# Kernel optimization log

Hardware: AMD Instinct MI355X
Metric: run time of the kernel (lower is better)

## Reference

```python
import jax, jax.numpy as jnp
import numpy as np

V = 500000
VD = 256
G = 4000
H = 8
GD = 256
HIDDEN = 128


def setup_inputs() -> dict:
    key = jax.random.key(0)
    ks = jax.random.split(key, 6)
    node_embeddings = jax.random.normal(ks[0], (V, VD), dtype=jnp.float32)
    node_to_graph_map = jnp.sort(jax.random.randint(ks[1], (V,), 0, G, dtype=jnp.int32))
    scale = lambda fan_in: 1.0 / np.sqrt(fan_in)
    scoring_w1 = jax.random.normal(ks[2], (VD, HIDDEN), dtype=jnp.float32) * scale(VD)
    scoring_w2 = jax.random.normal(ks[3], (HIDDEN, H), dtype=jnp.float32) * scale(HIDDEN)
    transform_w1 = jax.random.normal(ks[4], (VD, HIDDEN), dtype=jnp.float32) * scale(VD)
    transform_w2 = jax.random.normal(ks[5], (HIDDEN, GD), dtype=jnp.float32) * scale(HIDDEN)
    return {
        "node_embeddings": node_embeddings,
        "node_to_graph_map": node_to_graph_map,
        "num_graphs": G,
        "scoring_w1": scoring_w1,
        "scoring_w2": scoring_w2,
        "transform_w1": transform_w1,
        "transform_w2": transform_w2,
    }


def _segment_softmax(logits, segment_ids, num_segments):
    # logits: [V, H]; softmax over nodes within each graph, per head.
    seg_max = jax.ops.segment_max(logits, segment_ids, num_segments=num_segments)
    seg_max = jnp.where(jnp.isfinite(seg_max), seg_max, 0.0)
    exp = jnp.exp(logits - seg_max[segment_ids])
    denom = jax.ops.segment_sum(exp, segment_ids, num_segments=num_segments)
    return exp / denom[segment_ids]


def reference(node_embeddings, node_to_graph_map, num_graphs,
              scoring_w1, scoring_w2, transform_w1, transform_w2):
    # Scoring MLP (hidden ReLU, linear out, no biases): [V, H]
    scores = jax.nn.relu(node_embeddings @ scoring_w1) @ scoring_w2
    # Per-graph softmax weights, per head: [V, H]
    weights = _segment_softmax(scores, node_to_graph_map, num_graphs)
    # Transformation MLP, then the call() applies the activation to the MLP output.
    node_reprs = jax.nn.relu(jax.nn.relu(node_embeddings @ transform_w1) @ transform_w2)  # [V, GD]
    node_reprs = node_reprs.reshape(-1, H, GD // H)  # [V, H, GD/H]
    weighted = (weights[:, :, None] * node_reprs).reshape(-1, GD)  # [V, GD]
    graph_reprs = jax.ops.segment_sum(weighted, node_to_graph_map, num_segments=num_graphs)
    return graph_reprs
```

## Files before the change

### kernel.cpp

```cpp
#include <hip/hip_runtime.h>
#include <hip/hip_fp16.h>

#define VD 256
#define HID 128
#define GD 256
#define NH 8
#define NGRAPH 4000
#define RT 64
#define MAXROWS 512

typedef _Float16 f16;
typedef f16 f16x4 __attribute__((ext_vector_type(4)));
typedef f16 f16x8 __attribute__((ext_vector_type(8)));
typedef float f32x4 __attribute__((ext_vector_type(4)));

__device__ __forceinline__ f16x8 load_a_frag(const float* p) {
  float4 p0 = *(const float4*)(p);
  float4 p1 = *(const float4*)(p + 4);
  f16x8 v;
  v[0] = (f16)p0.x; v[1] = (f16)p0.y; v[2] = (f16)p0.z; v[3] = (f16)p0.w;
  v[4] = (f16)p1.x; v[5] = (f16)p1.y; v[6] = (f16)p1.z; v[7] = (f16)p1.w;
  return v;
}

__device__ __forceinline__ void pack_b_dev(const float* __restrict__ src,
                                           f16* __restrict__ dst,
                                           int K, int Nsrc, int Ndst, int t) {
  int NB = Ndst / 16, KB = K / 32;
  int total = KB * NB * 64;
  if (t >= total) return;
  int lane = t & 63;
  int frag = t >> 6;
  int nb = frag % NB, kb = frag / NB;
  int col = nb * 16 + (lane & 15);
  int krow = kb * 32 + (lane >> 4) * 8;
  f16x8 o;
  #pragma unroll
  for (int i = 0; i < 8; ++i) {
    float v = (col < Nsrc) ? src[(size_t)(krow + i) * Nsrc + col] : 0.0f;
    o[i] = (f16)v;
  }
  *(f16x8*)(dst + (size_t)t * 8) = o;
}

__global__ __launch_bounds__(256) void k_prep(
    const float* __restrict__ w1s, const float* __restrict__ w1t,
    const float* __restrict__ w2t, const float* __restrict__ w2s,
    const int* __restrict__ map,
    f16* __restrict__ W1sp, f16* __restrict__ W1tp,
    f16* __restrict__ W2tp, f16* __restrict__ W2sp,
    int* __restrict__ gs, int V, int G) {
  int b = blockIdx.x;
  int tid = threadIdx.x;
  if (b < 16) {
    pack_b_dev(w1s, W1sp, VD, HID, HID, b * 256 + tid);
  } else if (b < 32) {
    pack_b_dev(w1t, W1tp, VD, HID, HID, (b - 16) * 256 + tid);
  } else if (b < 48) {
    pack_b_dev(w2t, W2tp, HID, GD, GD, (b - 32) * 256 + tid);
  } else if (b == 48) {
    pack_b_dev(w2s, W2sp, HID, NH, 16, tid);
  } else {
    int g = (b - 49) * 256 + tid;
    if (g > G) return;
    int lo = 0, hi = V;
    while (lo < hi) {
      int mid = (lo + hi) >> 1;
      if (map[mid] < g) lo = mid + 1; else hi = mid;
    }
    gs[g] = lo;
  }
}

__global__ __attribute__((amdgpu_flat_work_group_size(512, 512),
                          amdgpu_waves_per_eu(4, 4))) void k_stage1(
    const float* __restrict__ E, int V, int ntiles,
    const f16* __restrict__ W1sp, const f16* __restrict__ W2sp,
    const f16* __restrict__ W1tp,
    float* __restrict__ scores, f16* __restrict__ ht) {
  __shared__ __attribute__((aligned(16))) f16 lE[RT][VD + 8];
  __shared__ __attribute__((aligned(16))) f16 lH[RT][HID + 8];
  __shared__ __attribute__((aligned(16))) f16 lT[RT][HID + 8];
  const int tid = threadIdx.x;
  const int wave = tid >> 6;
  const int lane = tid & 63;
  const int hi = lane >> 4;
  const int lo = lane & 15;
  const int srow = tid >> 6;
  const int scol = (tid & 63) * 4;

  f16x8 Bs[8], Bt[8];
  #pragma unroll
  for (int kb = 0; kb < 8; ++kb) {
    Bs[kb] = *(const f16x8*)(W1sp + ((size_t)(kb * 8 + wave) * 64 + lane) * 8);
    Bt[kb] = *(const f16x8*)(W1tp + ((size_t)(kb * 8 + wave) * 64 + lane) * 8);
  }

  int t = blockIdx.x;
  if (t >= ntiles) return;
  const int stride = gridDim.x;

  float4 pf[8];
  {
    const int r0 = t * RT;
    #pragma unroll
    for (int p = 0; p < 8; ++p) {
      int grow = r0 + p * 8 + srow;
      pf[p] = (grow < V) ? *(const float4*)(E + (size_t)grow * VD + scol)
                         : make_float4(0.f, 0.f, 0.f, 0.f);
    }
  }

  while (t < ntiles) {
    const int r0 = t * RT;
    #pragma unroll
    for (int p = 0; p < 8; ++p) {
      f16x4 h;
      h[0] = (f16)pf[p].x; h[1] = (f16)pf[p].y;
      h[2] = (f16)pf[p].z; h[3] = (f16)pf[p].w;
      *(f16x4*)&lE[p * 8 + srow][scol] = h;
    }
    const int tn = t + stride;
    if (tn < ntiles) {
      const int rn = tn * RT;
      #pragma unroll
      for (int p = 0; p < 8; ++p) {
        int grow = rn + p * 8 + srow;
        pf[p] = (grow < V) ? *(const float4*)(E + (size_t)grow * VD + scol)
                           : make_float4(0.f, 0.f, 0.f, 0.f);
      }
    }
    __syncthreads();

    #pragma unroll
    for (int m = 0; m < 4; ++m) {
      f32x4 as = {0.f, 0.f, 0.f, 0.f};
      f32x4 at = {0.f, 0.f, 0.f, 0.f};
      #pragma unroll
      for (int kb = 0; kb < 8; ++kb) {
        f16x8 a = *(const f16x8*)&lE[m * 16 + lo][kb * 32 + hi * 8];
        as = __builtin_amdgcn_mfma_f32_16x16x32_f16(a, Bs[kb], as, 0, 0, 0);
        at = __builtin_amdgcn_mfma_f32_16x16x32_f16(a, Bt[kb], at, 0, 0, 0);
      }
      #pragma unroll
      for (int r = 0; r < 4; ++r) {
        lH[m * 16 + hi * 4 + r][wave * 16 + lo] = (f16)fmaxf(as[r], 0.f);
        if (ht != nullptr)
          lT[m * 16 + hi * 4 + r][wave * 16 + lo] = (f16)fmaxf(at[r], 0.f);
      }
    }
    __syncthreads();

    if (ht != nullptr) {
      #pragma unroll
      for (int p = 0; p < 2; ++p) {
        int c = p * 512 + tid;
        int row = c >> 4;
        int col = (c & 15) * 8;
        int grow = r0 + row;
        if (grow < V)
          *(f16x8*)(ht + (size_t)grow * HID + col) = *(const f16x8*)&lT[row][col];
      }
    }

    if (wave < 4) {
      f16x8 a2[4];
      #pragma unroll
      for (int kb = 0; kb < 4; ++kb)
        a2[kb] = *(const f16x8*)&lH[wave * 16 + lo][kb * 32 + hi * 8];
      f32x4 acc = {0.f, 0.f, 0.f, 0.f};
      #pragma unroll
      for (int kb = 0; kb < 4; ++kb) {
        f16x8 b = *(const f16x8*)(W2sp + ((size_t)kb * 64 + lane) * 8);
        acc = __builtin_amdgcn_mfma_f32_16x16x32_f16(a2[kb], b, acc, 0, 0, 0);
      }
      if (lo < NH) {
        #pragma unroll
        for (int r = 0; r < 4; ++r) {
          int row = r0 + wave * 16 + hi * 4 + r;
          if (row < V) scores[(size_t)row * NH + lo] = acc[r];
        }
      }
    }
    t = tn;
  }
}

__global__ __attribute__((amdgpu_flat_work_group_size(256, 256),
                          amdgpu_waves_per_eu(4, 4))) void k_graph(
    const f16* __restrict__ ht, const float* __restrict__ scores,
    const f16* __restrict__ W2tp, const int* __restrict__ gs,
    float* __restrict__ out, int V) {
  __shared__ float red[4][NH];
  __shared__ float lW[MAXROWS * NH];
  const int g = blockIdx.x;
  const int tid = threadIdx.x;
  const int wave = tid >> 6;
  const int lane = tid & 63;
  const int hi = lane >> 4;
  const int lo = lane & 15;
  const int s = gs[g], e = gs[g + 1];
  const int n = e - s;

  if (n <= 0) {
    out[(size_t)g * GD + tid] = 0.f;
    return;
  }

  f16x8 b[4][4];
  #pragma unroll
  for (int j = 0; j < 4; ++j)
    #pragma unroll
    for (int kb = 0; kb < 4; ++kb)
      b[j][kb] = *(const f16x8*)(
          W2tp + ((size_t)(kb * 16 + wave * 4 + j) * 64 + lane) * 8);

  const int h0 = wave * 2, h1 = wave * 2 + 1;
  float m0, m1, ri0, ri1;
  const bool use_lds = (n <= MAXROWS);

  if (use_lds) {
    for (int c = tid; c < n * 2; c += 256)
      *(float4*)&lW[c * 4] = *(const float4*)(scores + (size_t)s * NH + c * 4);
    __syncthreads();

    float mx[NH];
    #pragma unroll
    for (int h = 0; h < NH; ++h) mx[h] = -1e30f;
    for (int i = tid; i < n; i += 256) {
      #pragma unroll
      for (int h = 0; h < NH; ++h) mx[h] = fmaxf(mx[h], lW[i * NH + h]);
    }
    #pragma unroll
    for (int off = 32; off >= 1; off >>= 1)
      #pragma unroll
      for (int h = 0; h < NH; ++h) mx[h] = fmaxf(mx[h], __shfl_xor(mx[h], off));
    if (lane == 0) {
      #pragma unroll
      for (int h = 0; h < NH; ++h) red[wave][h] = mx[h];
    }
    __syncthreads();
    #pragma unroll
    for (int h = 0; h < NH; ++h)
      mx[h] = fmaxf(fmaxf(red[0][h], red[1][h]), fmaxf(red[2][h], red[3][h]));
    __syncthreads();

    float sm[NH];
    #pragma unroll
    for (int h = 0; h < NH; ++h) sm[h] = 0.f;
    for (int i = tid; i < n; i += 256) {
      #pragma unroll
      for (int h = 0; h < NH; ++h) sm[h] += __expf(lW[i * NH + h] - mx[h]);
    }
    #pragma unroll
    for (int off = 32; off >= 1; off >>= 1)
      #pragma unroll
      for (int h = 0; h < NH; ++h) sm[h] += __shfl_xor(sm[h], off);
    if (lane == 0) {
      #pragma unroll
      for (int h = 0; h < NH; ++h) red[wave][h] = sm[h];
    }
    __syncthreads();

    float rinv[NH];
    #pragma unroll
    for (int h = 0; h < NH; ++h)
      rinv[h] = 1.f / (red[0][h] + red[1][h] + red[2][h] + red[3][h]);

    for (int i = tid; i < n; i += 256) {
      #pragma unroll
      for (int h = 0; h < NH; ++h)
        lW[i * NH + h] = __expf(lW[i * NH + h] - mx[h]) * rinv[h];
    }
    __syncthreads();
    m0 = mx[h0]; m1 = mx[h1]; ri0 = rinv[h0]; ri1 = rinv[h1];
  } else {
    float mx[NH];
    #pragma unroll
    for (int h = 0; h < NH; ++h) mx[h] = -1e30f;
    for (int i = s + tid; i < e; i += 256) {
      float4 s0 = *(const float4*)(scores + (size_t)i * NH);
      float4 s1 = *(const float4*)(scores + (size_t)i * NH + 4);
      mx[0] = fmaxf(mx[0], s0.x); mx[1] = fmaxf(mx[1], s0.y);
      mx[2] = fmaxf(mx[2], s0.z); mx[3] = fmaxf(mx[3], s0.w);
      mx[4] = fmaxf(mx[4], s1.x); mx[5] = fmaxf(mx[5], s1.y);
      mx[6] = fmaxf(mx[6], s1.z); mx[7] = fmaxf(mx[7], s1.w);
    }
    #pragma unroll
    for (int off = 32; off >= 1; off >>= 1)
      #pragma unroll
      for (int h = 0; h < NH; ++h) mx[h] = fmaxf(mx[h], __shfl_xor(mx[h], off));
    if (lane == 0) {
      #pragma unroll
      for (int h = 0; h < NH; ++h) red[wave][h] = mx[h];
    }
    __syncthreads();
    #pragma unroll
    for (int h = 0; h < NH; ++h)
      mx[h] = fmaxf(fmaxf(red[0][h], red[1][h]), fmaxf(red[2][h], red[3][h]));
    __syncthreads();

    float sm[NH];
    #pragma unroll
    for (int h = 0; h < NH; ++h) sm[h] = 0.f;
    for (int i = s + tid; i < e; i += 256) {
      float4 s0 = *(const float4*)(scores + (size_t)i * NH);
      float4 s1 = *(const float4*)(scores + (size_t)i * NH + 4);
      sm[0] += __expf(s0.x - mx[0]); sm[1] += __expf(s0.y - mx[1]);
      sm[2] += __expf(s0.z - mx[2]); sm[3] += __expf(s0.w - mx[3]);
      sm[4] += __expf(s1.x - mx[4]); sm[5] += __expf(s1.y - mx[5]);
      sm[6] += __expf(s1.z - mx[6]); sm[7] += __expf(s1.w - mx[7]);
    }
    #pragma unroll
    for (int off = 32; off >= 1; off >>= 1)
      #pragma unroll
      for (int h = 0; h < NH; ++h) sm[h] += __shfl_xor(sm[h], off);
    if (lane == 0) {
      #pragma unroll
      for (int h = 0; h < NH; ++h) red[wave][h] = sm[h];
    }
    __syncthreads();
    m0 = mx[h0]; m1 = mx[h1];
    ri0 = 1.f / (red[0][h0] + red[1][h0] + red[2][h0] + red[3][h0]);
    ri1 = 1.f / (red[0][h1] + red[1][h1] + red[2][h1] + red[3][h1]);
  }

  float vsum[4] = {0.f, 0.f, 0.f, 0.f};

  for (int cb = s; cb < e; cb += 16) {
    f16x8 a[4];
    int arow = cb + lo;
    int ar = arow < V ? arow : V - 1;
    #pragma unroll
    for (int kb = 0; kb < 4; ++kb)
      a[kb] = *(const f16x8*)(ht + (size_t)ar * HID + kb * 32 + hi * 8);

    int wr = cb + hi * 4;
    float wv[2][4];
    if (use_lds) {
      #pragma unroll
      for (int r = 0; r < 4; ++r) {
        int row = wr + r;
        bool in = row < e;
        int rel = in ? (row - s) : 0;
        wv[0][r] = in ? lW[rel * NH + h0] : 0.f;
        wv[1][r] = in ? lW[rel * NH + h1] : 0.f;
      }
    } else {
      #pragma unroll
      for (int r = 0; r < 4; ++r) {
        int row = wr + r;
        bool in = row < e;
        float sc0 = in ? scores[(size_t)row * NH + h0] : 0.f;
        float sc1 = in ? scores[(size_t)row * NH + h1] : 0.f;
        wv[0][r] = in ? __expf(sc0 - m0) * ri0 : 0.f;
        wv[1][r] = in ? __expf(sc1 - m1) * ri1 : 0.f;
      }
    }
    #pragma unroll
    for (int j = 0; j < 4; ++j) {
      f32x4 acc = {0.f, 0.f, 0.f, 0.f};
      #pragma unroll
      for (int kb = 0; kb < 4; ++kb)
        acc = __builtin_amdgcn_mfma_f32_16x16x32_f16(a[kb], b[j][kb], acc, 0, 0, 0);
      const float* wvp = wv[j >> 1];
      float v = 0.f;
      #pragma unroll
      for (int r = 0; r < 4; ++r) v += fmaxf(acc[r], 0.f) * wvp[r];
      vsum[j] += v;
    }
  }

  #pragma unroll
  for (int j = 0; j < 4; ++j) {
    float v = vsum[j];
    v += __shfl_xor(v, 16);
    v += __shfl_xor(v, 32);
    if (lane < 16) out[(size_t)g * GD + (wave * 4 + j) * 16 + lo] = v;
  }
}

__global__ __launch_bounds__(64) void k_stats(
    float* __restrict__ scores, const int* __restrict__ gs) {
  int g = blockIdx.x;
  int lane = threadIdx.x;
  int s = gs[g], e = gs[g + 1];
  if (e <= s) return;
  float mx[NH];
  #pragma unroll
  for (int h = 0; h < NH; ++h) mx[h] = -1e30f;
  for (int i = s + lane; i < e; i += 64) {
    float4 s0 = *(const float4*)(scores + (size_t)i * NH);
    float4 s1 = *(const float4*)(scores + (size_t)i * NH + 4);
    mx[0] = fmaxf(mx[0], s0.x); mx[1] = fmaxf(mx[1], s0.y);
    mx[2] = fmaxf(mx[2], s0.z); mx[3] = fmaxf(mx[3], s0.w);
    mx[4] = fmaxf(mx[4], s1.x); mx[5] = fmaxf(mx[5], s1.y);
    mx[6] = fmaxf(mx[6], s1.z); mx[7] = fmaxf(mx[7], s1.w);
  }
  #pragma unroll
  for (int off = 32; off >= 1; off >>= 1)
    #pragma unroll
    for (int h = 0; h < NH; ++h) mx[h] = fmaxf(mx[h], __shfl_xor(mx[h], off));
  float sm[NH];
  #pragma unroll
  for (int h = 0; h < NH; ++h) sm[h] = 0.f;
  for (int i = s + lane; i < e; i += 64) {
    float4 s0 = *(const float4*)(scores + (size_t)i * NH);
    float4 s1 = *(const float4*)(scores + (size_t)i * NH + 4);
    sm[0] += __expf(s0.x - mx[0]); sm[1] += __expf(s0.y - mx[1]);
    sm[2] += __expf(s0.z - mx[2]); sm[3] += __expf(s0.w - mx[3]);
    sm[4] += __expf(s1.x - mx[4]); sm[5] += __expf(s1.y - mx[5]);
    sm[6] += __expf(s1.z - mx[6]); sm[7] += __expf(s1.w - mx[7]);
  }
  #pragma unroll
  for (int off = 32; off >= 1; off >>= 1)
    #pragma unroll
    for (int h = 0; h < NH; ++h) sm[h] += __shfl_xor(sm[h], off);
  float rinv[NH];
  #pragma unroll
  for (int h = 0; h < NH; ++h) rinv[h] = 1.f / sm[h];
  for (int i = s + lane; i < e; i += 64) {
    float4 s0 = *(const float4*)(scores + (size_t)i * NH);
    float4 s1 = *(const float4*)(scores + (size_t)i * NH + 4);
    s0.x = __expf(s0.x - mx[0]) * rinv[0]; s0.y = __expf(s0.y - mx[1]) * rinv[1];
    s0.z = __expf(s0.z - mx[2]) * rinv[2]; s0.w = __expf(s0.w - mx[3]) * rinv[3];
    s1.x = __expf(s1.x - mx[4]) * rinv[4]; s1.y = __expf(s1.y - mx[5]) * rinv[5];
    s1.z = __expf(s1.z - mx[6]) * rinv[6]; s1.w = __expf(s1.w - mx[7]) * rinv[7];
    *(float4*)(scores + (size_t)i * NH) = s0;
    *(float4*)(scores + (size_t)i * NH + 4) = s1;
  }
}

__global__ __launch_bounds__(256, 2) void k_transform2(
    const float* __restrict__ E, int V,
    const f16* __restrict__ W1tp, const f16* __restrict__ W2tp,
    const float* __restrict__ w, const int* __restrict__ gs,
    float* __restrict__ out) {
  __shared__ f16 hl[16][HID + 8];
  const int g = blockIdx.x;
  const int wave = threadIdx.x >> 6;
  const int lane = threadIdx.x & 63;
  const int hi = lane >> 4;
  const int lo = lane & 15;
  const int s = gs[g], e = gs[g + 1];

  f16x8 b[4][4];
  #pragma unroll
  for (int j = 0; j < 4; ++j)
    #pragma unroll
    for (int kb = 0; kb < 4; ++kb)
      b[j][kb] = *(const f16x8*)(
          W2tp + ((size_t)(kb * 16 + wave * 4 + j) * 64 + lane) * 8);

  float vsum[4] = {0.f, 0.f, 0.f, 0.f};

  for (int cb = s; cb < e; cb += 16) {
    int arow = cb + lo;
    int ar = arow < V ? arow : V - 1;
    f16x8 a[8];
    const float* ep = E + (size_t)ar * VD + hi * 8;
    #pragma unroll
    for (int kb = 0; kb < 8; ++kb) a[kb] = load_a_frag(ep + kb * 32);

    __syncthreads();
    #pragma unroll
    for (int nn = 0; nn < 2; ++nn) {
      int n = wave * 2 + nn;
      f32x4 acc = {0.f, 0.f, 0.f, 0.f};
      #pragma unroll
      for (int kb = 0; kb < 8; ++kb) {
        f16x8 bb = *(const f16x8*)(W1tp + ((size_t)(kb * 8 + n) * 64 + lane) * 8);
        acc = __builtin_amdgcn_mfma_f32_16x16x32_f16(a[kb], bb, acc, 0, 0, 0);
      }
      #pragma unroll
      for (int r = 0; r < 4; ++r)
        hl[hi * 4 + r][n * 16 + lo] = (f16)fmaxf(acc[r], 0.f);
    }
    __syncthreads();

    int wr = cb + hi * 4;
    float wv[2][4];
    #pragma unroll
    for (int hh = 0; hh < 2; ++hh) {
      int head = wave * 2 + hh;
      #pragma unroll
      for (int r = 0; r < 4; ++r) {
        int row = wr + r;
        wv[hh][r] = (row < e) ? w[(size_t)row * NH + head] : 0.f;
      }
    }
    f16x8 a2[4];
    #pragma unroll
    for (int kb = 0; kb < 4; ++kb)
      a2[kb] = *(const f16x8*)&hl[lo][kb * 32 + hi * 8];
    #pragma unroll
    for (int j = 0; j < 4; ++j) {
      f32x4 acc = {0.f, 0.f, 0.f, 0.f};
      #pragma unroll
      for (int kb = 0; kb < 4; ++kb)
        acc = __builtin_amdgcn_mfma_f32_16x16x32_f16(a2[kb], b[j][kb], acc, 0, 0, 0);
      const float* wvp = wv[j >> 1];
      float v = 0.f;
      #pragma unroll
      for (int r = 0; r < 4; ++r) v += fmaxf(acc[r], 0.f) * wvp[r];
      vsum[j] += v;
    }
  }

  #pragma unroll
  for (int j = 0; j < 4; ++j) {
    float v = vsum[j];
    v += __shfl_xor(v, 16);
    v += __shfl_xor(v, 32);
    if (lane < 16) out[(size_t)g * GD + (wave * 4 + j) * 16 + lo] = v;
  }
}

extern "C" void kernel_launch(void* const* d_in, const int* in_sizes, int n_in,
                              void* d_out, int out_size, void* d_ws, size_t ws_size,
                              hipStream_t stream) {
  const float* E   = (const float*)d_in[0];
  const int*   map = (const int*)d_in[1];
  const float* w1s = (const float*)d_in[3];
  const float* w2s = (const float*)d_in[4];
  const float* w1t = (const float*)d_in[5];
  const float* w2t = (const float*)d_in[6];
  const int V = in_sizes[0] / VD;
  const int G = NGRAPH;

  char* ws = (char*)d_ws;
  size_t off = 0;
  float* scores = (float*)(ws + off); off += (size_t)V * NH * 4;
  int* gs = (int*)(ws + off); off += (size_t)(G + 1) * 4;
  off = (off + 255) & ~(size_t)255;
  f16* W1sp = (f16*)(ws + off); off += (size_t)VD * HID * 2;
  f16* W1tp = (f16*)(ws + off); off += (size_t)VD * HID * 2;
  f16* W2tp = (f16*)(ws + off); off += (size_t)HID * GD * 2;
  f16* W2sp = (f16*)(ws + off); off += (size_t)HID * 16 * 2;
  off = (off + 255) & ~(size_t)255;
  f16* ht = (f16*)(ws + off);
  const size_t need_fused = off + (size_t)V * HID * 2;
  const bool fused = ws_size >= need_fused;

  k_prep<<<65, 256, 0, stream>>>(w1s, w1t, w2t, w2s, map,
                                 W1sp, W1tp, W2tp, W2sp, gs, V, G);

  const int ntiles = (V + RT - 1) / RT;
  const int grid1 = (ntiles + 3) / 4;
  k_stage1<<<grid1, 512, 0, stream>>>(
      E, V, ntiles, W1sp, W2sp, W1tp, scores, fused ? ht : nullptr);

  if (fused) {
    k_graph<<<G, 256, 0, stream>>>(ht, scores, W2tp, gs, (float*)d_out, V);
  } else {
    k_stats<<<G, 64, 0, stream>>>(scores, gs);
    k_transform2<<<G, 256, 0, stream>>>(E, V, W1tp, W2tp, scores, gs,
                                        (float*)d_out);
  }
}
```

Baseline: 263.5 us.

## Widen per-graph kernel to 512 threads and overlap ht stores with scoring

The per-graph pooling kernel now runs 8 waves per block, one per head. Each wave owns 32 output columns and processes 32 node rows per iteration, where before 4 waves each covered two heads over 16 rows. In stage 1, the hidden-activation stores to ht move to the four otherwise idle waves, so they proceed while waves 0-3 compute the scores MFMA. The wider block halves the per-wave B-fragment registers, but each wave now reloads every ht row, which raises total L2 traffic per graph.

```diff
diff --git a/kernel.cpp b/kernel.cpp
--- a/kernel.cpp
+++ b/kernel.cpp
@@ -151,18 +151,6 @@
     }
     __syncthreads();
 
-    if (ht != nullptr) {
-      #pragma unroll
-      for (int p = 0; p < 2; ++p) {
-        int c = p * 512 + tid;
-        int row = c >> 4;
-        int col = (c & 15) * 8;
-        int grow = r0 + row;
-        if (grow < V)
-          *(f16x8*)(ht + (size_t)grow * HID + col) = *(const f16x8*)&lT[row][col];
-      }
-    }
-
     if (wave < 4) {
       f16x8 a2[4];
       #pragma unroll
@@ -181,17 +169,28 @@
           if (row < V) scores[(size_t)row * NH + lo] = acc[r];
         }
       }
+    } else if (ht != nullptr) {
+      const int base = tid - 256;
+      #pragma unroll
+      for (int p = 0; p < 4; ++p) {
+        int c = p * 256 + base;
+        int row = c >> 4;
+        int col = (c & 15) * 8;
+        int grow = r0 + row;
+        if (grow < V)
+          *(f16x8*)(ht + (size_t)grow * HID + col) = *(const f16x8*)&lT[row][col];
+      }
     }
     t = tn;
   }
 }
 
-__global__ __attribute__((amdgpu_flat_work_group_size(256, 256),
+__global__ __attribute__((amdgpu_flat_work_group_size(512, 512),
                           amdgpu_waves_per_eu(4, 4))) void k_graph(
     const f16* __restrict__ ht, const float* __restrict__ scores,
     const f16* __restrict__ W2tp, const int* __restrict__ gs,
     float* __restrict__ out, int V) {
-  __shared__ float red[4][NH];
+  __shared__ float red[8][NH];
   __shared__ float lW[MAXROWS * NH];
   const int g = blockIdx.x;
   const int tid = threadIdx.x;
@@ -203,31 +202,30 @@
   const int n = e - s;
 
   if (n <= 0) {
-    out[(size_t)g * GD + tid] = 0.f;
+    if (tid < GD) out[(size_t)g * GD + tid] = 0.f;
     return;
   }
 
-  f16x8 b[4][4];
-  #pragma unroll
-  for (int j = 0; j < 4; ++j)
+  f16x8 b[2][4];
+  #pragma unroll
+  for (int nb = 0; nb < 2; ++nb)
     #pragma unroll
     for (int kb = 0; kb < 4; ++kb)
-      b[j][kb] = *(const f16x8*)(
-          W2tp + ((size_t)(kb * 16 + wave * 4 + j) * 64 + lane) * 8);
-
-  const int h0 = wave * 2, h1 = wave * 2 + 1;
-  float m0, m1, ri0, ri1;
+      b[nb][kb] = *(const f16x8*)(
+          W2tp + ((size_t)(kb * 16 + wave * 2 + nb) * 64 + lane) * 8);
+
+  float mh, rih;
   const bool use_lds = (n <= MAXROWS);
 
   if (use_lds) {
-    for (int c = tid; c < n * 2; c += 256)
+    for (int c = tid; c < n * 2; c += 512)
       *(float4*)&lW[c * 4] = *(const float4*)(scores + (size_t)s * NH + c * 4);
     __syncthreads();
 
     float mx[NH];
     #pragma unroll
     for (int h = 0; h < NH; ++h) mx[h] = -1e30f;
-    for (int i = tid; i < n; i += 256) {
+    for (int i = tid; i < n; i += 512) {
       #pragma unroll
       for (int h = 0; h < NH; ++h) mx[h] = fmaxf(mx[h], lW[i * NH + h]);
     }
@@ -241,14 +239,19 @@
     }
     __syncthreads();
     #pragma unroll
-    for (int h = 0; h < NH; ++h)
-      mx[h] = fmaxf(fmaxf(red[0][h], red[1][h]), fmaxf(red[2][h], red[3][h]));
+    for (int h = 0; h < NH; ++h) {
+      float m01 = fmaxf(red[0][h], red[1][h]);
+      float m23 = fmaxf(red[2][h], red[3][h]);
+      float m45 = fmaxf(red[4][h], red[5][h]);
+      float m67 = fmaxf(red[6][h], red[7][h]);
+      mx[h] = fmaxf(fmaxf(m01, m23), fmaxf(m45, m67));
+    }
     __syncthreads();
 
     float sm[NH];
     #pragma unroll
     for (int h = 0; h < NH; ++h) sm[h] = 0.f;
-    for (int i = tid; i < n; i += 256) {
+    for (int i = tid; i < n; i += 512) {
       #pragma unroll
       for (int h = 0; h < NH; ++h) sm[h] += __expf(lW[i * NH + h] - mx[h]);
     }
@@ -265,20 +268,21 @@
     float rinv[NH];
     #pragma unroll
     for (int h = 0; h < NH; ++h)
-      rinv[h] = 1.f / (red[0][h] + red[1][h] + red[2][h] + red[3][h]);
-
-    for (int i = tid; i < n; i += 256) {
+      rinv[h] = 1.f / (red[0][h] + red[1][h] + red[2][h] + red[3][h] +
+                       red[4][h] + red[5][h] + red[6][h] + red[7][h]);
+
+    for (int i = tid; i < n; i += 512) {
       #pragma unroll
       for (int h = 0; h < NH; ++h)
         lW[i * NH + h] = __expf(lW[i * NH + h] - mx[h]) * rinv[h];
     }
     __syncthreads();
-    m0 = mx[h0]; m1 = mx[h1]; ri0 = rinv[h0]; ri1 = rinv[h1];
+    mh = mx[wave]; rih = rinv[wave];
   } else {
     float mx[NH];
     #pragma unroll
     for (int h = 0; h < NH; ++h) mx[h] = -1e30f;
-    for (int i = s + tid; i < e; i += 256) {
+    for (int i = s + tid; i < e; i += 512) {
       float4 s0 = *(const float4*)(scores + (size_t)i * NH);
       float4 s1 = *(const float4*)(scores + (size_t)i * NH + 4);
       mx[0] = fmaxf(mx[0], s0.x); mx[1] = fmaxf(mx[1], s0.y);
@@ -296,14 +300,19 @@
     }
     __syncthreads();
     #pragma unroll
-    for (int h = 0; h < NH; ++h)
-      mx[h] = fmaxf(fmaxf(red[0][h], red[1][h]), fmaxf(red[2][h], red[3][h]));
+    for (int h = 0; h < NH; ++h) {
+      float m01 = fmaxf(red[0][h], red[1][h]);
+      float m23 = fmaxf(red[2][h], red[3][h]);
+      float m45 = fmaxf(red[4][h], red[5][h]);
+      float m67 = fmaxf(red[6][h], red[7][h]);
+      mx[h] = fmaxf(fmaxf(m01, m23), fmaxf(m45, m67));
+    }
     __syncthreads();
 
     float sm[NH];
     #pragma unroll
     for (int h = 0; h < NH; ++h) sm[h] = 0.f;
-    for (int i = s + tid; i < e; i += 256) {
+    for (int i = s + tid; i < e; i += 512) {
       float4 s0 = *(const float4*)(scores + (size_t)i * NH);
       float4 s1 = *(const float4*)(scores + (size_t)i * NH + 4);
       sm[0] += __expf(s0.x - mx[0]); sm[1] += __expf(s0.y - mx[1]);
@@ -320,63 +329,71 @@
       for (int h = 0; h < NH; ++h) red[wave][h] = sm[h];
     }
     __syncthreads();
-    m0 = mx[h0]; m1 = mx[h1];
-    ri0 = 1.f / (red[0][h0] + red[1][h0] + red[2][h0] + red[3][h0]);
-    ri1 = 1.f / (red[0][h1] + red[1][h1] + red[2][h1] + red[3][h1]);
-  }
-
-  float vsum[4] = {0.f, 0.f, 0.f, 0.f};
-
-  for (int cb = s; cb < e; cb += 16) {
-    f16x8 a[4];
-    int arow = cb + lo;
-    int ar = arow < V ? arow : V - 1;
+    mh = mx[wave];
+    rih = 1.f / (red[0][wave] + red[1][wave] + red[2][wave] + red[3][wave] +
+                 red[4][wave] + red[5][wave] + red[6][wave] + red[7][wave]);
+  }
+
+  float vs0 = 0.f, vs1 = 0.f;
+
+  for (int cb = s; cb < e; cb += 32) {
+    f16x8 aA[4], aB[4];
+    int rA = cb + lo;       rA = rA < V ? rA : V - 1;
+    int rB = cb + 16 + lo;  rB = rB < V ? rB : V - 1;
     #pragma unroll
     for (int kb = 0; kb < 4; ++kb)
-      a[kb] = *(const f16x8*)(ht + (size_t)ar * HID + kb * 32 + hi * 8);
-
-    int wr = cb + hi * 4;
-    float wv[2][4];
+      aA[kb] = *(const f16x8*)(ht + (size_t)rA * HID + kb * 32 + hi * 8);
+    #pragma unroll
+    for (int kb = 0; kb < 4; ++kb)
+      aB[kb] = *(const f16x8*)(ht + (size_t)rB * HID + kb * 32 + hi * 8);
+
+    float wA[4], wB[4];
     if (use_lds) {
       #pragma unroll
       for (int r = 0; r < 4; ++r) {
-        int row = wr + r;
-        bool in = row < e;
-        int rel = in ? (row - s) : 0;
-        wv[0][r] = in ? lW[rel * NH + h0] : 0.f;
-        wv[1][r] = in ? lW[rel * NH + h1] : 0.f;
+        int rowA = cb + hi * 4 + r;
+        int rowB = rowA + 16;
+        wA[r] = (rowA < e) ? lW[(rowA - s) * NH + wave] : 0.f;
+        wB[r] = (rowB < e) ? lW[(rowB - s) * NH + wave] : 0.f;
       }
     } else {
       #pragma unroll
       for (int r = 0; r < 4; ++r) {
-        int row = wr + r;
-        bool in = row < e;
-        float sc0 = in ? scores[(size_t)row * NH + h0] : 0.f;
-        float sc1 = in ? scores[(size_t)row * NH + h1] : 0.f;
-        wv[0][r] = in ? __expf(sc0 - m0) * ri0 : 0.f;
-        wv[1][r] = in ? __expf(sc1 - m1) * ri1 : 0.f;
-      }
-    }
-    #pragma unroll
-    for (int j = 0; j < 4; ++j) {
-      f32x4 acc = {0.f, 0.f, 0.f, 0.f};
+        int rowA = cb + hi * 4 + r;
+        int rowB = rowA + 16;
+        wA[r] = (rowA < e) ? __expf(scores[(size_t)rowA * NH + wave] - mh) * rih
+                           : 0.f;
+        wB[r] = (rowB < e) ? __expf(scores[(size_t)rowB * NH + wave] - mh) * rih
+                           : 0.f;
+      }
+    }
+
+    #pragma unroll
+    for (int nb = 0; nb < 2; ++nb) {
+      f32x4 accA = {0.f, 0.f, 0.f, 0.f};
       #pragma unroll
       for (int kb = 0; kb < 4; ++kb)
-        acc = __builtin_amdgcn_mfma_f32_16x16x32_f16(a[kb], b[j][kb], acc, 0, 0, 0);
-      const float* wvp = wv[j >> 1];
+        accA = __builtin_amdgcn_mfma_f32_16x16x32_f16(aA[kb], b[nb][kb], accA, 0, 0, 0);
+      f32x4 accB = {0.f, 0.f, 0.f, 0.f};
+      #pragma unroll
+      for (int kb = 0; kb < 4; ++kb)
+        accB = __builtin_amdgcn_mfma_f32_16x16x32_f16(aB[kb], b[nb][kb], accB, 0, 0, 0);
       float v = 0.f;
       #pragma unroll
-      for (int r = 0; r < 4; ++r) v += fmaxf(acc[r], 0.f) * wvp[r];
-      vsum[j] += v;
-    }
-  }
-
-  #pragma unroll
-  for (int j = 0; j < 4; ++j) {
-    float v = vsum[j];
+      for (int r = 0; r < 4; ++r) v += fmaxf(accA[r], 0.f) * wA[r];
+      #pragma unroll
+      for (int r = 0; r < 4; ++r) v += fmaxf(accB[r], 0.f) * wB[r];
+      if (nb == 0) vs0 += v; else vs1 += v;
+    }
+  }
+
+  #pragma unroll
+  for (int nb = 0; nb < 2; ++nb) {
+    float v = (nb == 0) ? vs0 : vs1;
     v += __shfl_xor(v, 16);
     v += __shfl_xor(v, 32);
-    if (lane < 16) out[(size_t)g * GD + (wave * 4 + j) * 16 + lo] = v;
+    if (lane < 16)
+      out[(size_t)g * GD + wave * 32 + nb * 16 + lo] = v;
   }
 }
 
@@ -551,7 +568,7 @@
       E, V, ntiles, W1sp, W2sp, W1tp, scores, fused ? ht : nullptr);
 
   if (fused) {
-    k_graph<<<G, 256, 0, stream>>>(ht, scores, W2tp, gs, (float*)d_out, V);
+    k_graph<<<G, 512, 0, stream>>>(ht, scores, W2tp, gs, (float*)d_out, V);
   } else {
     k_stats<<<G, 64, 0, stream>>>(scores, gs);
     k_transform2<<<G, 256, 0, stream>>>(E, V, W1tp, W2tp, scores, gs,
```

New measurement: 341.0 us. 29.4% more time.
